# Kernel tuning notes

Hardware: AMD Instinct MI355X
Metric: run time of the kernel (lower is better)

## Reference

```python
import jax, jax.numpy as jnp
import numpy as np

S, B, D, F = 2048, 8, 1024, 4096
EPS = 1e-5

def setup_inputs() -> dict:
    key = jax.random.key(0)
    ks = jax.random.split(key, 16)
    sc = lambda fan_in: 1.0 / np.sqrt(fan_in)
    inp = {
        'src': jax.random.normal(ks[0], (S, B, D), dtype=jnp.float32),
        'wq': jax.random.uniform(ks[1], (D, D), jnp.float32, -sc(D), sc(D)),
        'bq': jnp.zeros((D,), jnp.float32),
        'wk': jax.random.uniform(ks[2], (D, D), jnp.float32, -sc(D), sc(D)),
        'bk': jnp.zeros((D,), jnp.float32),
        'wv': jax.random.uniform(ks[3], (D, D), jnp.float32, -sc(D), sc(D)),
        'bv': jnp.zeros((D,), jnp.float32),
        'wo': jax.random.uniform(ks[4], (D, D), jnp.float32, -sc(D), sc(D)),
        'bo': jnp.zeros((D,), jnp.float32),
        'w1': jax.random.uniform(ks[5], (F, D), jnp.float32, -sc(D), sc(D)),
        'b1': jnp.zeros((F,), jnp.float32),
        'w2': jax.random.uniform(ks[6], (D, F), jnp.float32, -sc(F), sc(F)),
        'b2': jnp.zeros((D,), jnp.float32),
        'g1': jnp.ones((D,), jnp.float32),
        'be1': jnp.zeros((D,), jnp.float32),
        'g2': jnp.ones((D,), jnp.float32),
        'be2': jnp.zeros((D,), jnp.float32),
    }
    return inp

def _layer_norm(x, g, b):
    mu = jnp.mean(x, axis=-1, keepdims=True)
    var = jnp.mean(jnp.square(x - mu), axis=-1, keepdims=True)
    return (x - mu) / jnp.sqrt(var + EPS) * g + b

def _forward(src, wq, bq, wk, bk, wv, bv, wo, bo, w1, b1, w2, b2, g1, be1, g2, be2):
    # Linear attention (ELU+1 feature map, no normalizer — faithful to source)
    Q = jax.nn.elu(src @ wq.T + bq) + 1.0  # [S,B,D]
    K = jax.nn.elu(src @ wk.T + bk) + 1.0  # [S,B,D]
    V = src @ wv.T + bv                    # [S,B,D]
    KV = jnp.einsum('sbd,sbe->bde', K, V)  # [B,D,D]
    attn = jnp.einsum('sbd,bde->sbe', Q, KV)  # [S,B,D]
    attn = attn @ wo.T + bo
    x = _layer_norm(src + attn, g1, be1)   # dropout is identity (p=0 / eval)
    ffn = jax.nn.relu(x @ w1.T + b1) @ w2.T + b2
    return _layer_norm(x + ffn, g2, be2)

def reference(src, wq, bq, wk, bk, wv, bv, wo, bo, w1, b1, w2, b2, g1, be1, g2, be2):
    return _forward(src, wq, bq, wk, bk, wv, bv, wo, bo, w1, b1, w2, b2, g1, be1, g2, be2)
```

## Files before the change

### kernel.cpp

```cpp
#include <hip/hip_runtime.h>
#include <hip/hip_bf16.h>
#include <math.h>


typedef __attribute__((ext_vector_type(8))) short short8;
typedef __attribute__((ext_vector_type(4))) short short4_t;
typedef __attribute__((ext_vector_type(4))) float f32x4;

#define S_DIM 2048
#define B_DIM 8
#define D_DIM 1024
#define F_DIM 4096

__device__ __forceinline__ unsigned short f2bf(float f) {
  __hip_bfloat16 h = __float2bfloat16(f);
  return *reinterpret_cast<unsigned short*>(&h);
}

#define GLD16(gp, sp)                                              \
  __builtin_amdgcn_global_load_lds(                                \
      (const __attribute__((address_space(1))) void*)(gp),         \
      (__attribute__((address_space(3))) void*)(sp), 16, 0, 0)

#define BAR()                                  \
  do {                                         \
    asm volatile("" ::: "memory");             \
    __builtin_amdgcn_s_barrier();              \
    asm volatile("" ::: "memory");             \
  } while (0)
#define WAITVM10() asm volatile("s_waitcnt vmcnt(10)" ::: "memory")
#define WAITVM0() asm volatile("s_waitcnt vmcnt(0)" ::: "memory")
#define SCHED_FENCE() __builtin_amdgcn_sched_barrier(0)

template <int EPI>
__global__ __launch_bounds__(512, 2) void gemm256_kernel(
    const unsigned short* __restrict__ A, long lda, long sA,
    const unsigned short* __restrict__ B, long ldb, long sB,
    void* __restrict__ Cv, long ldc, long sC,
    const float* __restrict__ bias,
    const float* __restrict__ resid, long ldr, long sR, int K) {
  __shared__ short lds[65536];
  const int gx = gridDim.x;
  const int nwg = gx * gridDim.y;
  const int orig = blockIdx.y * gx + blockIdx.x;
  const int cpx = nwg >> 3;
  const int wgid = (orig & 7) * cpx + (orig >> 3);
  const int bx = wgid % gx, by = wgid / gx;
  const int bz = blockIdx.z;
  const unsigned short* Ablk = A + (long)bz * sA + (long)by * 256 * lda;
  const unsigned short* Bblk = B + (long)bz * sB + (long)bx * 256 * ldb;

  const int tid = threadIdx.x;
  const int w = tid >> 6, lane = tid & 63;
  const int wm = w >> 2, wn = w & 3;
  const int lr = lane & 15, kh = lane >> 4;

  const int sr = w * 8 + (lane >> 3);
  const int sc = ((lane & 7) ^ (lane >> 3)) * 8;
  const long aoff0 = (long)sr * lda + sc;
  const long aoff1 = (long)(128 + sr) * lda + sc;
  const int br0 = sr + ((sr >> 5) << 5);
  const int br1 = (64 + sr) + (((64 + sr) >> 5) << 5);
  const long boff0 = (long)br0 * ldb + sc;
  const long boff1 = (long)br1 * ldb + sc;
  const int dst0 = w * 1024;
  const int dst1 = (8 + w) * 1024;

#define STAGE_A(bufOff, h, kt)                                                \
  do {                                                                        \
    const unsigned short* _g = Ablk + (long)(h) * 64 * lda + (long)(kt) * 64; \
    GLD16(_g + aoff0, (char*)lds + (bufOff) + (h)*16384 + dst0);              \
    GLD16(_g + aoff1, (char*)lds + (bufOff) + (h)*16384 + dst1);              \
  } while (0)
#define STAGE_B(bufOff, nh, kt)                                               \
  do {                                                                        \
    const unsigned short* _g = Bblk + (long)(nh) * 32 * ldb + (long)(kt) * 64;\
    GLD16(_g + boff0, (char*)lds + (bufOff) + 32768 + (nh)*16384 + dst0);     \
    GLD16(_g + boff1, (char*)lds + (bufOff) + 32768 + (nh)*16384 + dst1);     \
  } while (0)

  const int chk0 = ((kh ^ (lr & 7)) << 4);
  const int chk1 = (((4 + kh) ^ (lr & 7)) << 4);
  const int aRdBase = (wm * 64 + lr) * 128;
  const int bRdBase = (wn * 32 + lr) * 128;

  short8 af[4][2], b0r[2][2], b1r[2][2];
  f32x4 acc[8][4];
#pragma unroll
  for (int m = 0; m < 8; ++m)
#pragma unroll
    for (int n = 0; n < 4; ++n)
#pragma unroll
      for (int j = 0; j < 4; ++j) acc[m][n][j] = 0.f;

#define LDA_H(bufOff, h)                                                     \
  do {                                                                       \
    const char* _p = (const char*)lds + (bufOff) + (h)*16384 + aRdBase;      \
    _Pragma("unroll") for (int m = 0; m < 4; ++m) {                          \
      af[m][0] = *(const short8*)(_p + m * 2048 + chk0);                     \
      af[m][1] = *(const short8*)(_p + m * 2048 + chk1);                     \
    }                                                                        \
  } while (0)
#define LDB_H(dst, bufOff, nh)                                               \
  do {                                                                       \
    const char* _p = (const char*)lds + (bufOff) + 32768 + (nh)*16384 + bRdBase; \
    _Pragma("unroll") for (int n = 0; n < 2; ++n) {                          \
      dst[n][0] = *(const short8*)(_p + n * 2048 + chk0);                    \
      dst[n][1] = *(const short8*)(_p + n * 2048 + chk1);                    \
    }                                                                        \
  } while (0)
#define MFMA_Q(mh, nh, bset)                                                 \
  do {                                                                       \
    SCHED_FENCE();                                                           \
    __builtin_amdgcn_s_setprio(1);                                           \
    _Pragma("unroll") for (int m = 0; m < 4; ++m)                            \
    _Pragma("unroll") for (int n = 0; n < 2; ++n)                            \
    _Pragma("unroll") for (int ks = 0; ks < 2; ++ks)                         \
      acc[(mh)*4 + m][(nh)*2 + n] = __builtin_amdgcn_mfma_f32_16x16x32_bf16( \
          af[m][ks], bset[n][ks], acc[(mh)*4 + m][(nh)*2 + n], 0, 0, 0);     \
    __builtin_amdgcn_s_setprio(0);                                           \
    SCHED_FENCE();                                                           \
  } while (0)

  const int T = K >> 6;
  STAGE_A(0, 0, 0); STAGE_B(0, 0, 0); STAGE_B(0, 1, 0); STAGE_A(0, 1, 0);
  STAGE_A(65536, 0, 1); STAGE_B(65536, 0, 1); STAGE_B(65536, 1, 1);
  WAITVM10(); BAR();

  for (int i = 0; i < (T >> 1); ++i) {
    const int kto  = 2 * i + 1;
    const int kte2 = (2 * i + 2 < T) ? (2 * i + 2) : (T - 1);
    const int kto2 = (2 * i + 3 < T) ? (2 * i + 3) : (T - 1);
    LDA_H(0, 0); LDB_H(b0r, 0, 0); STAGE_A(65536, 1, kto);
    WAITVM10(); BAR(); MFMA_Q(0, 0, b0r); BAR();
    LDB_H(b1r, 0, 1); STAGE_A(0, 0, kte2);
    WAITVM10(); BAR(); MFMA_Q(0, 1, b1r); BAR();
    LDA_H(0, 1); STAGE_B(0, 0, kte2);
    BAR(); MFMA_Q(1, 1, b1r); BAR();
    STAGE_B(0, 1, kte2);
    WAITVM10(); BAR(); MFMA_Q(1, 0, b0r); BAR();
    LDA_H(65536, 0); LDB_H(b0r, 65536, 0); STAGE_A(0, 1, kte2);
    WAITVM10(); BAR(); MFMA_Q(0, 0, b0r); BAR();
    LDB_H(b1r, 65536, 1); STAGE_A(65536, 0, kto2);
    WAITVM10(); BAR(); MFMA_Q(0, 1, b1r); BAR();
    LDA_H(65536, 1); STAGE_B(65536, 0, kto2);
    BAR(); MFMA_Q(1, 1, b1r); BAR();
    STAGE_B(65536, 1, kto2);
    WAITVM10(); BAR(); MFMA_Q(1, 0, b0r); BAR();
  }
  WAITVM0();

  const long gm0 = (long)by * 256 + wm * 128;
  const long gn0 = (long)bx * 256 + wn * 64;
  if constexpr (EPI == 4) {
    float* C = (float*)Cv + (long)bz * sC;
    const float* R = resid + (long)bz * sR;
#pragma unroll
    for (int mg = 0; mg < 8; ++mg)
#pragma unroll
      for (int ng = 0; ng < 4; ++ng) {
        const long col = gn0 + ng * 16 + lr;
        const float bcol = bias[col];
#pragma unroll
        for (int j = 0; j < 4; ++j) {
          const long row = gm0 + mg * 16 + kh * 4 + j;
          C[row * ldc + col] = acc[mg][ng][j] + bcol + R[row * ldr + col];
        }
      }
  } else {
    unsigned short* C = (unsigned short*)Cv + (long)bz * sC;
    const bool do_elu = (EPI == 5) && (gn0 < 2048);
#pragma unroll
    for (int mg = 0; mg < 8; ++mg)
#pragma unroll
      for (int ng = 0; ng < 4; ++ng) {
        const long col = gn0 + ng * 16 + lr;
        const float bcol = bias[col];
#pragma unroll
        for (int j = 0; j < 4; ++j) {
          const long row = gm0 + mg * 16 + kh * 4 + j;
          float v = acc[mg][ng][j] + bcol;
          if constexpr (EPI == 3) v = fmaxf(v, 0.f);
          if constexpr (EPI == 5) {
            if (do_elu) v = (v > 0.f) ? (v + 1.f) : expf(v);
          }
          C[row * ldc + col] = f2bf(v);
        }
      }
  }
#undef STAGE_A
#undef STAGE_B
#undef LDA_H
#undef LDB_H
#undef MFMA_Q
}

template <int EPI>
__global__ __launch_bounds__(256, 2) void gemm_bt_kernel(
    const unsigned short* __restrict__ A, long lda, long sA,
    const unsigned short* __restrict__ B, long ldb, long sB,
    void* __restrict__ Cv, long ldc, long sC,
    const float* __restrict__ bias,
    const float* __restrict__ resid, long ldr, long sR, int K) {
  __shared__ short As[128 * 32];
  __shared__ short Bs[128 * 32];
  const int gx = gridDim.x;
  const int nwg = gx * gridDim.y;
  const int orig = blockIdx.y * gx + blockIdx.x;
  const int cpx = nwg >> 3;
  const int wgid = (orig & 7) * cpx + (orig >> 3);
  const int bx = wgid % gx;
  const int by = wgid / gx;

  const int bz = blockIdx.z;
  const unsigned short* Ab = A + (long)bz * sA + (long)by * 128 * lda;
  const unsigned short* Bb = B + (long)bz * sB + (long)bx * 128 * ldb;
  const int tid = threadIdx.x;
  const int w = tid >> 6, lane = tid & 63;
  const int srow = lane >> 2;
  const int scol = (lane & 3) * 8;
  const int wr = (w >> 1) * 64, wc = (w & 1) * 64;
  const int lr = lane & 15, kh = lane >> 4;

  f32x4 acc[4][4];
#pragma unroll
  for (int m = 0; m < 4; ++m)
#pragma unroll
    for (int n = 0; n < 4; ++n)
#pragma unroll
      for (int j = 0; j < 4; ++j) acc[m][n][j] = 0.f;

  const unsigned short* ga0 = Ab + (long)(w * 16 + srow) * lda + scol;
  const unsigned short* ga1 = Ab + (long)(64 + w * 16 + srow) * lda + scol;
  const unsigned short* gb0 = Bb + (long)(w * 16 + srow) * ldb + scol;
  const unsigned short* gb1 = Bb + (long)(64 + w * 16 + srow) * ldb + scol;
  short* la0 = &As[(w * 16) * 32];
  short* la1 = &As[(64 + w * 16) * 32];
  short* lb0 = &Bs[(w * 16) * 32];
  short* lb1 = &Bs[(64 + w * 16) * 32];

  for (int k0 = 0; k0 < K; k0 += 32) {
    GLD16(ga0 + k0, la0);
    GLD16(ga1 + k0, la1);
    GLD16(gb0 + k0, lb0);
    GLD16(gb1 + k0, lb1);
    __syncthreads();
    short8 af[4], bf[4];
#pragma unroll
    for (int m = 0; m < 4; ++m)
      af[m] = *(const short8*)&As[(wr + m * 16 + lr) * 32 + kh * 8];
#pragma unroll
    for (int n = 0; n < 4; ++n)
      bf[n] = *(const short8*)&Bs[(wc + n * 16 + lr) * 32 + kh * 8];
#pragma unroll
    for (int m = 0; m < 4; ++m)
#pragma unroll
      for (int n = 0; n < 4; ++n)
        acc[m][n] =
            __builtin_amdgcn_mfma_f32_16x16x32_bf16(af[m], bf[n], acc[m][n], 0, 0, 0);
    __syncthreads();
  }

  const long gm0 = (long)by * 128 + wr;
  const long gn0 = (long)bx * 128 + wc;
  unsigned short* C = (unsigned short*)Cv + (long)bz * sC;
#pragma unroll
  for (int m = 0; m < 4; ++m)
#pragma unroll
    for (int n = 0; n < 4; ++n) {
      const long col = gn0 + n * 16 + lr;
#pragma unroll
      for (int j = 0; j < 4; ++j) {
        const long row = gm0 + m * 16 + kh * 4 + j;
        C[row * ldc + col] = f2bf(acc[m][n][j]);
      }
    }
}

__global__ __launch_bounds__(256) void transpose_kernel(
    const unsigned short* __restrict__ in, unsigned short* __restrict__ out,
    long ld) {
  __shared__ unsigned short t[64][68];
  const int b = blockIdx.z;
  const long s0 = (long)blockIdx.x * 64, d0 = (long)blockIdx.y * 64;
  const int tid = threadIdx.x;
  {
    const int r = tid >> 3, c = (tid & 7) * 8;
#pragma unroll
    for (int it = 0; it < 2; ++it) {
      const int s = r + it * 32;
      const unsigned short* g = &in[((s0 + s) * B_DIM + b) * ld + d0 + c];
      short4_t v0 = *(const short4_t*)g;
      short4_t v1 = *(const short4_t*)(g + 4);
      *(short4_t*)&t[s][c] = v0;
      *(short4_t*)&t[s][c + 4] = v1;
    }
  }
  __syncthreads();
  {
    const int d = tid >> 3, c = (tid & 7) * 8;
#pragma unroll
    for (int it = 0; it < 2; ++it) {
      const int dd = d + it * 32;
      short8 v;
#pragma unroll
      for (int j = 0; j < 8; ++j) v[j] = (short)t[c + j][dd];
      *(short8*)&out[(long)b * ((long)D_DIM * S_DIM) + (d0 + dd) * S_DIM + s0 + c] = v;
    }
  }
}

template <int WRITE_BF16>
__global__ __launch_bounds__(256) void layernorm_kernel(
    const float* in, float* outf, unsigned short* __restrict__ outb,
    const float* __restrict__ gamma, const float* __restrict__ beta) {
  const long row = blockIdx.x;
  const float* x = in + row * D_DIM;
  const int tid = threadIdx.x;
  const int lane = tid & 63, w = tid >> 6;
  f32x4 v = *(const f32x4*)&x[tid * 4];
  float s = v[0] + v[1] + v[2] + v[3];
  float q = v[0] * v[0] + v[1] * v[1] + v[2] * v[2] + v[3] * v[3];
#pragma unroll
  for (int off = 32; off > 0; off >>= 1) {
    s += __shfl_down(s, off, 64);
    q += __shfl_down(q, off, 64);
  }
  __shared__ float red[8];
  if (lane == 0) { red[w] = s; red[w + 4] = q; }
  __syncthreads();
  s = red[0] + red[1] + red[2] + red[3];
  q = red[4] + red[5] + red[6] + red[7];
  const float mu = s * (1.f / D_DIM);
  const float var = q * (1.f / D_DIM) - mu * mu;
  const float rs = rsqrtf(var + 1e-5f);
  f32x4 g = *(const f32x4*)&gamma[tid * 4];
  f32x4 bb = *(const f32x4*)&beta[tid * 4];
  f32x4 o;
#pragma unroll
  for (int j = 0; j < 4; ++j) o[j] = (v[j] - mu) * rs * g[j] + bb[j];
  *(f32x4*)&outf[row * D_DIM + tid * 4] = o;
  if constexpr (WRITE_BF16) {
    short4_t ob;
#pragma unroll
    for (int j = 0; j < 4; ++j) ob[j] = (short)f2bf(o[j]);
    *(short4_t*)&outb[row * D_DIM + tid * 4] = ob;
  }
}

__global__ __launch_bounds__(256) void cast_kernel(
    const float* __restrict__ in, unsigned short* __restrict__ out, long n) {
  long i = ((long)blockIdx.x * 256 + threadIdx.x) * 8;
  if (i >= n) return;
  f32x4 a = *(const f32x4*)&in[i];
  f32x4 b = *(const f32x4*)&in[i + 4];
  short8 v;
#pragma unroll
  for (int j = 0; j < 4; ++j) v[j] = (short)f2bf(a[j]);
#pragma unroll
  for (int j = 0; j < 4; ++j) v[4 + j] = (short)f2bf(b[j]);
  *(short8*)&out[i] = v;
}

extern "C" void kernel_launch(void* const* d_in, const int* in_sizes, int n_in,
                              void* d_out, int out_size, void* d_ws, size_t ws_size,
                              hipStream_t stream) {
  const float* src = (const float*)d_in[0];
  const float* wq  = (const float*)d_in[1];
  const float* bq  = (const float*)d_in[2];
  const float* wk  = (const float*)d_in[3];
  const float* bk  = (const float*)d_in[4];
  const float* wv  = (const float*)d_in[5];
  const float* bv  = (const float*)d_in[6];
  const float* wo  = (const float*)d_in[7];
  const float* bo  = (const float*)d_in[8];
  const float* w1  = (const float*)d_in[9];
  const float* b1  = (const float*)d_in[10];
  const float* w2  = (const float*)d_in[11];
  const float* b2  = (const float*)d_in[12];
  const float* g1  = (const float*)d_in[13];
  const float* be1 = (const float*)d_in[14];
  const float* g2  = (const float*)d_in[15];
  const float* be2 = (const float*)d_in[16];

  const long MB = 1024L * 1024L;
  if (ws_size < 248 * MB) return;
  char* ws = (char*)d_ws;
  unsigned short* w1b   = (unsigned short*)(ws + 0 * MB);
  unsigned short* w2b   = (unsigned short*)(ws + 8 * MB);
  unsigned short* srcb  = (unsigned short*)(ws + 16 * MB);
  unsigned short* Kt    = (unsigned short*)(ws + 16 * MB);
  unsigned short* Vt    = (unsigned short*)(ws + 48 * MB);
  float*          AO    = (float*)(ws + 16 * MB);
  float*          X     = (float*)(ws + 16 * MB);
  unsigned short* KVm   = (unsigned short*)(ws + 80 * MB);
  unsigned short* Mt    = (unsigned short*)(ws + 96 * MB);
  unsigned short* Xb    = (unsigned short*)(ws + 80 * MB);
  unsigned short* wqkvb = (unsigned short*)(ws + 112 * MB);
  float*          bqkv  = (float*)(ws + 118 * MB);
  unsigned short* wob   = (unsigned short*)(ws + 119 * MB);
  unsigned short* QKVb  = (unsigned short*)(ws + 144 * MB);
  unsigned short* H     = (unsigned short*)(ws + 112 * MB);

  const dim3 blk(256);
  const dim3 blk512(512);
  cast_kernel<<<dim3(512), blk, 0, stream>>>(wq, wqkvb, 1048576);
  cast_kernel<<<dim3(512), blk, 0, stream>>>(wk, wqkvb + 1048576, 1048576);
  cast_kernel<<<dim3(512), blk, 0, stream>>>(wv, wqkvb + 2097152, 1048576);
  cast_kernel<<<dim3(512), blk, 0, stream>>>(wo, wob, 1048576);
  cast_kernel<<<dim3(2048), blk, 0, stream>>>(w1, w1b, 4194304);
  cast_kernel<<<dim3(2048), blk, 0, stream>>>(w2, w2b, 4194304);
  cast_kernel<<<dim3(8192), blk, 0, stream>>>(src, srcb, 16777216);
  hipMemcpyAsync(bqkv, bq, 4096, hipMemcpyDeviceToDevice, stream);
  hipMemcpyAsync(bqkv + 1024, bk, 4096, hipMemcpyDeviceToDevice, stream);
  hipMemcpyAsync(bqkv + 2048, bv, 4096, hipMemcpyDeviceToDevice, stream);

  gemm256_kernel<5><<<dim3(12, 64, 1), blk512, 0, stream>>>(
      srcb, 1024, 0, wqkvb, 1024, 0, QKVb, 3072, 0, bqkv, nullptr, 0, 0, 1024);

  transpose_kernel<<<dim3(32, 16, 8), blk, 0, stream>>>(QKVb + 1024, Kt, 3072);
  transpose_kernel<<<dim3(32, 16, 8), blk, 0, stream>>>(QKVb + 2048, Vt, 3072);

  gemm_bt_kernel<0><<<dim3(8, 8, 8), blk, 0, stream>>>(
      Kt, 2048, 2097152, Vt, 2048, 2097152, KVm, 1024, 1048576,
      nullptr, nullptr, 0, 0, 2048);
  gemm_bt_kernel<0><<<dim3(8, 8, 8), blk, 0, stream>>>(
      wob, 1024, 0, KVm, 1024, 1048576, Mt, 1024, 1048576,
      nullptr, nullptr, 0, 0, 1024);
  gemm256_kernel<4><<<dim3(4, 8, 8), blk512, 0, stream>>>(
      QKVb, 24576, 3072, Mt, 1024, 1048576, AO, 8192, 1024,
      bo, src, 8192, 1024, 1024);

  layernorm_kernel<1><<<dim3(16384), blk, 0, stream>>>(AO, X, Xb, g1, be1);

  gemm256_kernel<3><<<dim3(16, 64, 1), blk512, 0, stream>>>(
      Xb, 1024, 0, w1b, 1024, 0, H, 4096, 0, b1, nullptr, 0, 0, 1024);
  gemm256_kernel<4><<<dim3(4, 64, 1), blk512, 0, stream>>>(
      H, 4096, 0, w2b, 4096, 0, (float*)d_out, 1024, 0,
      b2, X, 1024, 0, 4096);

  layernorm_kernel<0><<<dim3(16384), blk, 0, stream>>>(
      (float*)d_out, (float*)d_out, nullptr, g2, be2);
}
```

Baseline: 652.5 us.

## Replace fine-grained interleaved GEMM pipeline with simple double-buffered k-loop

Replaces the hand-interleaved 8-phase main loop, where each quarter of MFMAs was fenced by barriers and paired with a partial stage load, with a plain per-k-tile loop. Each iteration computes all four MFMA quarters from one LDS buffer, then refills that buffer with tile t+2 and waits with vmcnt(8). It also drops the sched_barrier fences and the s_setprio raises around MFMA blocks. This cuts barrier count and lets the compiler schedule freely, but loses the fine overlap of global-to-LDS loads with MFMA work within a tile.

```diff
diff --git a/kernel.cpp b/kernel.cpp
--- a/kernel.cpp
+++ b/kernel.cpp
@@ -28,9 +28,8 @@
     __builtin_amdgcn_s_barrier();              \
     asm volatile("" ::: "memory");             \
   } while (0)
-#define WAITVM10() asm volatile("s_waitcnt vmcnt(10)" ::: "memory")
+#define WAITVM8() asm volatile("s_waitcnt vmcnt(8)" ::: "memory")
 #define WAITVM0() asm volatile("s_waitcnt vmcnt(0)" ::: "memory")
-#define SCHED_FENCE() __builtin_amdgcn_sched_barrier(0)
 
 template <int EPI>
 __global__ __launch_bounds__(512, 2) void gemm256_kernel(
@@ -111,44 +110,39 @@
   } while (0)
 #define MFMA_Q(mh, nh, bset)                                                 \
   do {                                                                       \
-    SCHED_FENCE();                                                           \
-    __builtin_amdgcn_s_setprio(1);                                           \
     _Pragma("unroll") for (int m = 0; m < 4; ++m)                            \
     _Pragma("unroll") for (int n = 0; n < 2; ++n)                            \
     _Pragma("unroll") for (int ks = 0; ks < 2; ++ks)                         \
       acc[(mh)*4 + m][(nh)*2 + n] = __builtin_amdgcn_mfma_f32_16x16x32_bf16( \
           af[m][ks], bset[n][ks], acc[(mh)*4 + m][(nh)*2 + n], 0, 0, 0);     \
-    __builtin_amdgcn_s_setprio(0);                                           \
-    SCHED_FENCE();                                                           \
   } while (0)
 
   const int T = K >> 6;
   STAGE_A(0, 0, 0); STAGE_B(0, 0, 0); STAGE_B(0, 1, 0); STAGE_A(0, 1, 0);
   STAGE_A(65536, 0, 1); STAGE_B(65536, 0, 1); STAGE_B(65536, 1, 1);
-  WAITVM10(); BAR();
-
-  for (int i = 0; i < (T >> 1); ++i) {
-    const int kto  = 2 * i + 1;
-    const int kte2 = (2 * i + 2 < T) ? (2 * i + 2) : (T - 1);
-    const int kto2 = (2 * i + 3 < T) ? (2 * i + 3) : (T - 1);
-    LDA_H(0, 0); LDB_H(b0r, 0, 0); STAGE_A(65536, 1, kto);
-    WAITVM10(); BAR(); MFMA_Q(0, 0, b0r); BAR();
-    LDB_H(b1r, 0, 1); STAGE_A(0, 0, kte2);
-    WAITVM10(); BAR(); MFMA_Q(0, 1, b1r); BAR();
-    LDA_H(0, 1); STAGE_B(0, 0, kte2);
-    BAR(); MFMA_Q(1, 1, b1r); BAR();
-    STAGE_B(0, 1, kte2);
-    WAITVM10(); BAR(); MFMA_Q(1, 0, b0r); BAR();
-    LDA_H(65536, 0); LDB_H(b0r, 65536, 0); STAGE_A(0, 1, kte2);
-    WAITVM10(); BAR(); MFMA_Q(0, 0, b0r); BAR();
-    LDB_H(b1r, 65536, 1); STAGE_A(65536, 0, kto2);
-    WAITVM10(); BAR(); MFMA_Q(0, 1, b1r); BAR();
-    LDA_H(65536, 1); STAGE_B(65536, 0, kto2);
-    BAR(); MFMA_Q(1, 1, b1r); BAR();
-    STAGE_B(65536, 1, kto2);
-    WAITVM10(); BAR(); MFMA_Q(1, 0, b0r); BAR();
-  }
-  WAITVM0();
+  STAGE_A(65536, 1, 1);
+  WAITVM8();
+  BAR();
+
+  for (int t = 0; t < T; ++t) {
+    const int bo = (t & 1) ? 65536 : 0;
+    LDA_H(bo, 0); LDB_H(b0r, bo, 0);
+    MFMA_Q(0, 0, b0r);
+    LDB_H(b1r, bo, 1);
+    MFMA_Q(0, 1, b1r);
+    LDA_H(bo, 1);
+    MFMA_Q(1, 1, b1r);
+    MFMA_Q(1, 0, b0r);
+    BAR();
+    if (t + 2 < T) {
+      STAGE_A(bo, 0, t + 2); STAGE_B(bo, 0, t + 2);
+      STAGE_B(bo, 1, t + 2); STAGE_A(bo, 1, t + 2);
+      WAITVM8();
+    } else {
+      WAITVM0();
+    }
+    BAR();
+  }
 
   const long gm0 = (long)by * 256 + wm * 128;
   const long gn0 = (long)bx * 256 + wn * 64;
```

Measured after the change: 659.4 us. No clear change (+1.1%).
